# Kernel tuning notes

Hardware: AMD Instinct MI355X
Metric: run time of the kernel (lower is better)

The kernel has to match this reference:

```python
import jax, jax.numpy as jnp
import numpy as np

MAX_FLOW = 80.0
STEPS = 200
STEP_SIZE = 10.0
EPS = 1e-5
NOISE_STD = 0.05
GRAD_CLIP = 0.03


def _energy(flow, img1, img2, log_weights):
    # flow: (B,2,H,W), img1/img2: (B,3,H,W); returns per-sample energy (B,)
    _, _, H, W = img1.shape
    flow = flow * MAX_FLOW
    img1 = (img1 + 1.0) / 2.0
    img2 = (img2 + 1.0) / 2.0
    A = jnp.sum((img1 - img2) ** 2, axis=1)                       # (B,H,W)
    data_term = jnp.sum(jnp.sqrt(A + EPS), axis=(1, 2))           # (B,)
    # kernel_dx/_dy are per-channel [-1,1] finite differences -> slicing
    dx = flow[:, :, :, 1:] - flow[:, :, :, :-1]                   # (B,2,H,W-1)
    dy = flow[:, :, 1:, :] - flow[:, :, :-1, :]                   # (B,2,H-1,W)
    Bx = jnp.pad(jnp.sum(dx ** 2, axis=1), ((0, 0), (0, 0), (0, 1)))
    By = jnp.pad(jnp.sum(dy ** 2, axis=1), ((0, 0), (0, 1), (0, 0)))
    smooth_term = jnp.sum(jnp.sqrt(Bx + By + EPS), axis=(1, 2))   # (B,)
    out = jnp.exp(log_weights[0]) * data_term + jnp.exp(log_weights[1]) * smooth_term
    return out / (H * W)


def _langevin_sample(init, img2, log_weights, key):
    # 200-step Langevin MCMC: noise inject, clamp, energy grad, clipped update, clamp
    def energy_sum(x):
        flow, img1 = x[:, :2], x[:, 2:]
        return jnp.sum(_energy(flow, img1, img2, log_weights))

    grad_fn = jax.grad(energy_sum)

    def step(x, k):
        noise = NOISE_STD * jax.random.normal(k, x.shape, x.dtype)
        x = jnp.clip(x + noise, -1.0, 1.0)
        g = jnp.clip(grad_fn(x), -GRAD_CLIP, GRAD_CLIP)
        x = jnp.clip(x - STEP_SIZE * g, -1.0, 1.0)
        return x, None

    keys = jax.random.split(key, STEPS)
    x, _ = jax.lax.scan(step, init, keys)
    return x


def setup_inputs() -> dict:
    key = jax.random.key(0)
    k1, k2, k3, k4 = jax.random.split(key, 4)
    B, H, W = 8, 384, 512
    target1 = jax.random.normal(k1, (B, 2, H, W), dtype=jnp.float32)
    input1 = jax.random.uniform(k2, (B, 3, H, W), dtype=jnp.float32)
    input2 = jax.random.uniform(k3, (B, 3, H, W), dtype=jnp.float32)
    init = jax.random.uniform(k4, (B, 5, H, W), dtype=jnp.float32) * 2.0 - 1.0
    log_weights = jnp.ones((2,), dtype=jnp.float32)
    return {"target1": target1, "input1": input1, "input2": input2,
            "init": init, "log_weights": log_weights}


def reference(target1, input1, input2, init, log_weights):
    flow_pos = target1 / MAX_FLOW
    img1_pos = input1 * 2.0 - 1.0
    img2 = input2 * 2.0 - 1.0
    # negative samples via Langevin MCMC; detached as in the torch module
    neg = jax.lax.stop_gradient(_langevin_sample(init, img2, log_weights, jax.random.key(1)))
    flow_neg, img1_neg = neg[:, :2], neg[:, 2:]
    pos_energy = _energy(flow_pos, img1_pos, img2, log_weights)
    neg_energy = _energy(flow_neg, img1_neg, img2, log_weights)
    energies = jnp.stack([pos_energy, neg_energy])  # (2,B)
    return energies, flow_neg * MAX_FLOW, (img1_neg + 1.0) / 2.0
```

## Files before the change

### kernel.cpp

```cpp
#include <hip/hip_runtime.h>
#include <math.h>

#define HH 384
#define WW 512
#define HW 196608
#define HHW 98304
#define CHW 983040
#define NTOT 7864320
#define FLOW_N 3145728
#define OUT_FLOW_OFF 16
#define OUT_IMG_OFF (16 + FLOW_N)
#define EPS_F 1e-5f
#define EPS_S (1e-5f / 6400.0f)
#define INV_HW (1.0f/196608.0f)

__device__ __forceinline__ float rsq_f(float x)  { return __builtin_amdgcn_rsqf(x); }
__device__ __forceinline__ float ln_f(float x)   { return 0.69314718055994531f * __builtin_amdgcn_logf(x); }
__device__ __forceinline__ float sqrt_f(float x) { return __builtin_amdgcn_sqrtf(x); }

__host__ __device__ __forceinline__ void tf2x32(unsigned k0, unsigned k1,
                                                unsigned x0, unsigned x1,
                                                unsigned& o0, unsigned& o1) {
  const unsigned ks2 = k0 ^ k1 ^ 0x1BD11BDAu;
  x0 += k0; x1 += k1;
#define TFR(r) x0 += x1; x1 = (x1 << (r)) | (x1 >> (32 - (r))); x1 ^= x0;
  TFR(13) TFR(15) TFR(26) TFR(6)
  x0 += k1;  x1 += ks2 + 1u;
  TFR(17) TFR(29) TFR(16) TFR(24)
  x0 += ks2; x1 += k0 + 2u;
  TFR(13) TFR(15) TFR(26) TFR(6)
  x0 += k0;  x1 += k1 + 3u;
  TFR(17) TFR(29) TFR(16) TFR(24)
  x0 += k1;  x1 += ks2 + 4u;
  TFR(13) TFR(15) TFR(26) TFR(6)
  x0 += ks2; x1 += k0 + 5u;
#undef TFR
  o0 = x0; o1 = x1;
}

__device__ __forceinline__ float noise_from_bits(unsigned bits) {
  const float LO = -0.99999994f;
  float f = __uint_as_float((bits >> 9) | 0x3F800000u) - 1.0f;
  float u = fmaxf(LO, f * 2.0f + LO);
  float w = -ln_f((1.0f - u) * (1.0f + u));
  float p;
  if (w < 5.0f) {
    w -= 2.5f;
    p = 2.81022636e-08f;
    p = p * w + 3.43273939e-07f;
    p = p * w + -3.5233877e-06f;
    p = p * w + -4.39150654e-06f;
    p = p * w + 0.00021858087f;
    p = p * w + -0.00125372503f;
    p = p * w + -0.00417768164f;
    p = p * w + 0.246640727f;
    p = p * w + 1.50140941f;
  } else {
    w = sqrt_f(w) - 3.0f;
    p = -0.000200214257f;
    p = p * w + 0.000100950558f;
    p = p * w + 0.00134934322f;
    p = p * w + -0.00367342844f;
    p = p * w + 0.00573950773f;
    p = p * w + -0.0076224613f;
    p = p * w + 0.00943887047f;
    p = p * w + 1.00167406f;
    p = p * w + 2.83297682f;
  }
  float z = 1.4142135623730951f * (p * u);
  return 0.05f * z;
}

__device__ __forceinline__ float upd(float x, float g) {
  g = fminf(fmaxf(g, -0.03f), 0.03f);
  return fminf(fmaxf(x - 10.0f * g, -1.0f), 1.0f);
}

__device__ __forceinline__ void noise_store2(float* dst, const float xn[2],
                                             unsigned ka, unsigned kb, unsigned idx0) {
  unsigned o0, o1, o2, o3;
  tf2x32(ka, kb, 0u, idx0, o0, o1);
  tf2x32(ka, kb, 0u, idx0 + 1u, o2, o3);
  float r0 = fminf(fmaxf(xn[0] + noise_from_bits(o0 ^ o1), -1.0f), 1.0f);
  float r1 = fminf(fmaxf(xn[1] + noise_from_bits(o2 ^ o3), -1.0f), 1.0f);
  *(float2*)dst = make_float2(r0, r1);
}

__global__ void k_init(double* acc, float* sw, const float* lw) {
  int t = threadIdx.x;
  if (t < 32) acc[t] = 0.0;
  if (t == 32) {
    sw[0] = expf(lw[0]) * INV_HW * 0.5f;
    sw[1] = expf(lw[1]) * INV_HW * 80.0f;
  }
}

__global__ __launch_bounds__(256) void k_noise0(const float* __restrict__ init,
    float* __restrict__ Y, unsigned ka, unsigned kb) {
  int idx = blockIdx.x * 256 + threadIdx.x;
  unsigned o0, o1;
  tf2x32(ka, kb, 0u, (unsigned)idx, o0, o1);
  float nz = noise_from_bits(o0 ^ o1);
  Y[idx] = fminf(fmaxf(init[idx] + nz, -1.0f), 1.0f);
}

template <bool FINAL>
__global__ __launch_bounds__(256, 8) void k_step2(const float* __restrict__ X,
    float* __restrict__ Y, const float* __restrict__ in2,
    const float* __restrict__ sw, unsigned ka, unsigned kb) {
  int tid = blockIdx.x * 256 + threadIdx.x;
  int b = tid / HHW;
  int q = tid - b * HHW;
  int p = q * 2;
  int h = p >> 9, w = p & 511;
  float s0 = sw[0], s1 = sw[1];
  const float* F0 = X + b * CHW;
  const float* F1 = F0 + HW;
  const bool wpos = (w > 0), wend = (w == 510);
  const bool hpos = (h > 0), hlast = (h == 383);

  float cf[2][3], fm1[2], dw[2][2], dwm1[2], uf[2][3];
  {
    float2 a0 = *(const float2*)(F0 + p);
    float2 a1 = *(const float2*)(F1 + p);
    cf[0][0] = a0.x; cf[0][1] = a0.y;
    cf[1][0] = a1.x; cf[1][1] = a1.y;
    cf[0][2] = wend ? cf[0][1] : F0[p + 2];
    cf[1][2] = wend ? cf[1][1] : F1[p + 2];
    fm1[0] = wpos ? F0[p - 1] : cf[0][0];
    fm1[1] = wpos ? F1[p - 1] : cf[1][0];
    if (!hlast) {
      float2 d0 = *(const float2*)(F0 + p + WW);
      float2 d1 = *(const float2*)(F1 + p + WW);
      dw[0][0] = d0.x; dw[0][1] = d0.y;
      dw[1][0] = d1.x; dw[1][1] = d1.y;
      dwm1[0] = wpos ? F0[p + WW - 1] : fm1[0];
      dwm1[1] = wpos ? F1[p + WW - 1] : fm1[1];
    } else {
#pragma unroll
      for (int c = 0; c < 2; ++c) {
        dw[c][0] = cf[c][0]; dw[c][1] = cf[c][1];
        dwm1[c] = fm1[c];
      }
    }
    if (hpos) {
      float2 u0 = *(const float2*)(F0 + p - WW);
      float2 u1 = *(const float2*)(F1 + p - WW);
      uf[0][0] = u0.x; uf[0][1] = u0.y;
      uf[1][0] = u1.x; uf[1][1] = u1.y;
      uf[0][2] = wend ? uf[0][1] : F0[p - WW + 2];
      uf[1][2] = wend ? uf[1][1] : F1[p - WW + 2];
    } else {
#pragma unroll
      for (int c = 0; c < 2; ++c)
        for (int j = 0; j < 3; ++j) uf[c][j] = cf[c][j];
    }
  }

  float dxc[2][2], dyc[2][2], invSc[2], dxu[2][2], dyu[2][2], invSu[2];
  float dxl[2], dyl[2], invSL;
#pragma unroll
  for (int j = 0; j < 2; ++j) {
#pragma unroll
    for (int c = 0; c < 2; ++c) {
      dxc[c][j] = cf[c][j + 1] - cf[c][j];
      dyc[c][j] = dw[c][j] - cf[c][j];
      dxu[c][j] = uf[c][j + 1] - uf[c][j];
      dyu[c][j] = cf[c][j] - uf[c][j];
    }
    invSc[j] = rsq_f(dxc[0][j]*dxc[0][j] + dxc[1][j]*dxc[1][j]
                   + dyc[0][j]*dyc[0][j] + dyc[1][j]*dyc[1][j] + EPS_S);
    invSu[j] = rsq_f(dxu[0][j]*dxu[0][j] + dxu[1][j]*dxu[1][j]
                   + dyu[0][j]*dyu[0][j] + dyu[1][j]*dyu[1][j] + EPS_S);
  }
  dxl[0] = cf[0][0] - fm1[0];  dxl[1] = cf[1][0] - fm1[1];
  dyl[0] = dwm1[0] - fm1[0];   dyl[1] = dwm1[1] - fm1[1];
  invSL = rsq_f(dxl[0]*dxl[0] + dxl[1]*dxl[1]
              + dyl[0]*dyl[0] + dyl[1]*dyl[1] + EPS_S);

  float xnF[2][2];
#pragma unroll
  for (int j = 0; j < 2; ++j) {
#pragma unroll
    for (int c = 0; c < 2; ++c) {
      float g = -(dxc[c][j] + dyc[c][j]) * invSc[j];
      if (j == 0) { if (wpos) g += dxl[c] * invSL; }
      else        { g += dxc[c][0] * invSc[0]; }
      if (hpos)   { g += dyu[c][j] * invSu[j]; }
      xnF[c][j] = upd(cf[c][j], g * s1);
    }
  }

  const float* XI = F0 + 2 * HW;
  const float* I2 = in2 + b * 3 * HW;
  float xv[3][2], dI[3][2];
#pragma unroll
  for (int c = 0; c < 3; ++c) {
    float2 xvv = *(const float2*)(XI + c * HW + p);
    float2 ivv = *(const float2*)(I2 + c * HW + p);
    xv[c][0] = xvv.x; xv[c][1] = xvv.y;
    dI[c][0] = (xvv.x + 1.0f) * 0.5f - ((ivv.x * 2.0f - 1.0f) + 1.0f) * 0.5f;
    dI[c][1] = (xvv.y + 1.0f) * 0.5f - ((ivv.y * 2.0f - 1.0f) + 1.0f) * 0.5f;
  }
  float xnI[3][2];
#pragma unroll
  for (int j = 0; j < 2; ++j) {
    float A = dI[0][j]*dI[0][j] + dI[1][j]*dI[1][j] + dI[2][j]*dI[2][j];
    float sI = s0 * rsq_f(A + EPS_F);
#pragma unroll
    for (int c = 0; c < 3; ++c) xnI[c][j] = upd(xv[c][j], dI[c][j] * sI);
  }

  if (!FINAL) {
    int base = b * CHW + p;
    noise_store2(Y + base,      xnF[0], ka, kb, (unsigned)base);
    noise_store2(Y + base + HW, xnF[1], ka, kb, (unsigned)(base + HW));
#pragma unroll
    for (int c = 0; c < 3; ++c)
      noise_store2(Y + base + (2 + c) * HW, xnI[c], ka, kb,
                   (unsigned)(base + (2 + c) * HW));
  } else {
    float* outF = Y + OUT_FLOW_OFF + b * 2 * HW;
    *(float2*)(outF + p)      = make_float2(xnF[0][0]*80.f, xnF[0][1]*80.f);
    *(float2*)(outF + HW + p) = make_float2(xnF[1][0]*80.f, xnF[1][1]*80.f);
    float* outI = Y + OUT_IMG_OFF + b * 3 * HW;
#pragma unroll
    for (int c = 0; c < 3; ++c)
      *(float2*)(outI + c * HW + p) = make_float2((xnI[c][0]+1.f)*0.5f,
                                                  (xnI[c][1]+1.f)*0.5f);
  }
}

__device__ __forceinline__ void block_acc2(double v0, double v1, double* a0, double* a1) {
  for (int off = 32; off > 0; off >>= 1) {
    v0 += __shfl_down(v0, off, 64);
    v1 += __shfl_down(v1, off, 64);
  }
  __shared__ double s0m[4], s1m[4];
  int lane = threadIdx.x & 63, wv = threadIdx.x >> 6;
  if (lane == 0) { s0m[wv] = v0; s1m[wv] = v1; }
  __syncthreads();
  if (threadIdx.x == 0) {
    atomicAdd(a0, s0m[0] + s0m[1] + s0m[2] + s0m[3]);
    atomicAdd(a1, s1m[0] + s1m[1] + s1m[2] + s1m[3]);
  }
}

__global__ __launch_bounds__(256) void k_pos_energy(const float* __restrict__ t1,
    const float* __restrict__ in1, const float* __restrict__ in2,
    double* __restrict__ acc) {
  int blk = blockIdx.x;
  int b = blk / 96;
  int local = blk - b * 96;
  const float* T0 = t1 + b * 2 * HW;
  const float* T1 = T0 + HW;
  const float* I1 = in1 + b * 3 * HW;
  const float* I2 = in2 + b * 3 * HW;
  double data = 0.0, smooth = 0.0;
  for (int it = 0; it < 8; ++it) {
    int p = (local * 8 + it) * 256 + threadIdx.x;
    int h = p >> 9, w = p & 511;
    float f00 = (T0[p] / 80.0f) * 80.0f;
    float f10 = (T1[p] / 80.0f) * 80.0f;
    float dx0 = 0, dx1 = 0, dy0 = 0, dy1 = 0;
    if (w < 511) { dx0 = (T0[p+1]/80.0f)*80.0f - f00;  dx1 = (T1[p+1]/80.0f)*80.0f - f10; }
    if (h < 383) { dy0 = (T0[p+WW]/80.0f)*80.0f - f00; dy1 = (T1[p+WW]/80.0f)*80.0f - f10; }
    smooth += (double)sqrtf(dx0*dx0 + dx1*dx1 + dy0*dy0 + dy1*dy1 + EPS_F);
    float d0 = ((I1[p]*2.0f-1.0f)+1.0f)*0.5f        - ((I2[p]*2.0f-1.0f)+1.0f)*0.5f;
    float d1 = ((I1[p+HW]*2.0f-1.0f)+1.0f)*0.5f     - ((I2[p+HW]*2.0f-1.0f)+1.0f)*0.5f;
    float d2 = ((I1[p+2*HW]*2.0f-1.0f)+1.0f)*0.5f   - ((I2[p+2*HW]*2.0f-1.0f)+1.0f)*0.5f;
    data += (double)sqrtf(d0*d0 + d1*d1 + d2*d2 + EPS_F);
  }
  block_acc2(data, smooth, &acc[b], &acc[8 + b]);
}

__global__ __launch_bounds__(256) void k_neg_energy(const float* __restrict__ out,
    const float* __restrict__ in2, double* __restrict__ acc) {
  int blk = blockIdx.x;
  int b = blk / 96;
  int local = blk - b * 96;
  const float* F0 = out + OUT_FLOW_OFF + b * 2 * HW;
  const float* F1 = F0 + HW;
  const float* I = out + OUT_IMG_OFF + b * 3 * HW;
  const float* I2 = in2 + b * 3 * HW;
  double data = 0.0, smooth = 0.0;
  for (int it = 0; it < 8; ++it) {
    int p = (local * 8 + it) * 256 + threadIdx.x;
    int h = p >> 9, w = p & 511;
    float f00 = F0[p], f10 = F1[p];
    float dx0 = 0, dx1 = 0, dy0 = 0, dy1 = 0;
    if (w < 511) { dx0 = F0[p + 1] - f00;  dx1 = F1[p + 1] - f10; }
    if (h < 383) { dy0 = F0[p + WW] - f00; dy1 = F1[p + WW] - f10; }
    smooth += (double)sqrtf(dx0*dx0 + dx1*dx1 + dy0*dy0 + dy1*dy1 + EPS_F);
    float d0 = I[p]        - ((I2[p]*2.0f-1.0f)+1.0f)*0.5f;
    float d1 = I[p+HW]     - ((I2[p+HW]*2.0f-1.0f)+1.0f)*0.5f;
    float d2 = I[p+2*HW]   - ((I2[p+2*HW]*2.0f-1.0f)+1.0f)*0.5f;
    data += (double)sqrtf(d0*d0 + d1*d1 + d2*d2 + EPS_F);
  }
  block_acc2(data, smooth, &acc[16 + b], &acc[24 + b]);
}

__global__ void k_finalize(const double* __restrict__ acc,
                           const float* __restrict__ lw, float* __restrict__ out) {
  int t = threadIdx.x;
  if (t < 16) {
    int b = t & 7, neg = t >> 3;
    double data   = acc[neg * 16 + b];
    double smooth = acc[neg * 16 + 8 + b];
    double e0 = exp((double)lw[0]), e1 = exp((double)lw[1]);
    out[t] = (float)((e0 * data + e1 * smooth) / 196608.0);
  }
}

extern "C" void kernel_launch(void* const* d_in, const int* in_sizes, int n_in,
                              void* d_out, int out_size, void* d_ws, size_t ws_size,
                              hipStream_t stream) {
  const float* t1  = (const float*)d_in[0];
  const float* in1 = (const float*)d_in[1];
  const float* in2 = (const float*)d_in[2];
  const float* init = (const float*)d_in[3];
  const float* lw  = (const float*)d_in[4];
  float* out = (float*)d_out;

  double* acc = (double*)d_ws;
  float* sw = (float*)((char*)d_ws + 256);
  size_t need = 2048 + (size_t)NTOT * sizeof(float);
  float* bufA = (ws_size >= need) ? (float*)((char*)d_ws + 2048)
                                  : (float*)d_in[3];
  float* bufE = out + OUT_FLOW_OFF;

  unsigned K0[200], K1[200];
  for (int t = 0; t < 200; ++t) tf2x32(0u, 1u, 0u, (unsigned)t, K0[t], K1[t]);

  k_init<<<1, 64, 0, stream>>>(acc, sw, lw);
  k_pos_energy<<<8 * 96, 256, 0, stream>>>(t1, in1, in2, acc);
  k_noise0<<<NTOT / 256, 256, 0, stream>>>(init, bufE, K0[0], K1[0]);
  for (int t = 0; t < 199; ++t) {
    const float* src = (t % 2 == 0) ? bufE : bufA;
    float* dst       = (t % 2 == 0) ? bufA : bufE;
    k_step2<false><<<8 * HHW / 256, 256, 0, stream>>>(src, dst, in2, sw,
                                                      K0[t + 1], K1[t + 1]);
  }
  k_step2<true><<<8 * HHW / 256, 256, 0, stream>>>(bufA, out, in2, sw, 0u, 0u);
  k_neg_energy<<<8 * 96, 256, 0, stream>>>(out, in2, acc);
  k_finalize<<<1, 64, 0, stream>>>(acc, lw, out);
}
```

Baseline: 5.519 ms.

## Split pointwise image channels into a single fused 200-step kernel

The image channels' energy gradient is purely per-pixel, so all 200 Langevin steps for those three channels now run inside one kernel that keeps the values in registers. Only the two flow channels, which need a stencil, still ping-pong through global memory with one launch per step. This removes most of the per-step global traffic, which previously covered five channels plus in2. The image kernel runs long per thread with serial RNG work, and the ws fallback now writes to the output flow region.

```diff
diff --git a/kernel.cpp b/kernel.cpp
--- a/kernel.cpp
+++ b/kernel.cpp
@@ -76,13 +76,16 @@
   return fminf(fmaxf(x - 10.0f * g, -1.0f), 1.0f);
 }
 
+__device__ __forceinline__ float noise_at(unsigned ka, unsigned kb, unsigned idx) {
+  unsigned o0, o1;
+  tf2x32(ka, kb, 0u, idx, o0, o1);
+  return noise_from_bits(o0 ^ o1);
+}
+
 __device__ __forceinline__ void noise_store2(float* dst, const float xn[2],
                                              unsigned ka, unsigned kb, unsigned idx0) {
-  unsigned o0, o1, o2, o3;
-  tf2x32(ka, kb, 0u, idx0, o0, o1);
-  tf2x32(ka, kb, 0u, idx0 + 1u, o2, o3);
-  float r0 = fminf(fmaxf(xn[0] + noise_from_bits(o0 ^ o1), -1.0f), 1.0f);
-  float r1 = fminf(fmaxf(xn[1] + noise_from_bits(o2 ^ o3), -1.0f), 1.0f);
+  float r0 = fminf(fmaxf(xn[0] + noise_at(ka, kb, idx0), -1.0f), 1.0f);
+  float r1 = fminf(fmaxf(xn[1] + noise_at(ka, kb, idx0 + 1u), -1.0f), 1.0f);
   *(float2*)dst = make_float2(r0, r1);
 }
 
@@ -95,26 +98,27 @@
   }
 }
 
-__global__ __launch_bounds__(256) void k_noise0(const float* __restrict__ init,
+__global__ __launch_bounds__(256) void k_fnoise0(const float* __restrict__ init,
     float* __restrict__ Y, unsigned ka, unsigned kb) {
-  int idx = blockIdx.x * 256 + threadIdx.x;
-  unsigned o0, o1;
-  tf2x32(ka, kb, 0u, (unsigned)idx, o0, o1);
-  float nz = noise_from_bits(o0 ^ o1);
-  Y[idx] = fminf(fmaxf(init[idx] + nz, -1.0f), 1.0f);
+  int e = blockIdx.x * 256 + threadIdx.x;
+  int b = e / (2 * HW);
+  int r = e - b * 2 * HW;
+  int orig = b * CHW + r;
+  float nz = noise_at(ka, kb, (unsigned)orig);
+  Y[e] = fminf(fmaxf(init[orig] + nz, -1.0f), 1.0f);
 }
 
 template <bool FINAL>
-__global__ __launch_bounds__(256, 8) void k_step2(const float* __restrict__ X,
-    float* __restrict__ Y, const float* __restrict__ in2,
-    const float* __restrict__ sw, unsigned ka, unsigned kb) {
+__global__ __launch_bounds__(256, 8) void k_fstep(const float* __restrict__ X,
+    float* __restrict__ Y, const float* __restrict__ sw,
+    unsigned ka, unsigned kb) {
   int tid = blockIdx.x * 256 + threadIdx.x;
   int b = tid / HHW;
   int q = tid - b * HHW;
   int p = q * 2;
   int h = p >> 9, w = p & 511;
-  float s0 = sw[0], s1 = sw[1];
-  const float* F0 = X + b * CHW;
+  float s1 = sw[1];
+  const float* F0 = X + b * 2 * HW;
   const float* F1 = F0 + HW;
   const bool wpos = (w > 0), wend = (w == 510);
   const bool hpos = (h > 0), hlast = (h == 383);
@@ -191,44 +195,58 @@
     }
   }
 
-  const float* XI = F0 + 2 * HW;
-  const float* I2 = in2 + b * 3 * HW;
-  float xv[3][2], dI[3][2];
-#pragma unroll
-  for (int c = 0; c < 3; ++c) {
-    float2 xvv = *(const float2*)(XI + c * HW + p);
-    float2 ivv = *(const float2*)(I2 + c * HW + p);
-    xv[c][0] = xvv.x; xv[c][1] = xvv.y;
-    dI[c][0] = (xvv.x + 1.0f) * 0.5f - ((ivv.x * 2.0f - 1.0f) + 1.0f) * 0.5f;
-    dI[c][1] = (xvv.y + 1.0f) * 0.5f - ((ivv.y * 2.0f - 1.0f) + 1.0f) * 0.5f;
-  }
-  float xnI[3][2];
-#pragma unroll
-  for (int j = 0; j < 2; ++j) {
-    float A = dI[0][j]*dI[0][j] + dI[1][j]*dI[1][j] + dI[2][j]*dI[2][j];
-    float sI = s0 * rsq_f(A + EPS_F);
-#pragma unroll
-    for (int c = 0; c < 3; ++c) xnI[c][j] = upd(xv[c][j], dI[c][j] * sI);
-  }
-
   if (!FINAL) {
-    int base = b * CHW + p;
-    noise_store2(Y + base,      xnF[0], ka, kb, (unsigned)base);
-    noise_store2(Y + base + HW, xnF[1], ka, kb, (unsigned)(base + HW));
-#pragma unroll
-    for (int c = 0; c < 3; ++c)
-      noise_store2(Y + base + (2 + c) * HW, xnI[c], ka, kb,
-                   (unsigned)(base + (2 + c) * HW));
+    int nbase = b * CHW + p;
+    int sb = b * 2 * HW + p;
+    noise_store2(Y + sb,      xnF[0], ka, kb, (unsigned)nbase);
+    noise_store2(Y + sb + HW, xnF[1], ka, kb, (unsigned)(nbase + HW));
   } else {
     float* outF = Y + OUT_FLOW_OFF + b * 2 * HW;
     *(float2*)(outF + p)      = make_float2(xnF[0][0]*80.f, xnF[0][1]*80.f);
     *(float2*)(outF + HW + p) = make_float2(xnF[1][0]*80.f, xnF[1][1]*80.f);
-    float* outI = Y + OUT_IMG_OFF + b * 3 * HW;
-#pragma unroll
-    for (int c = 0; c < 3; ++c)
-      *(float2*)(outI + c * HW + p) = make_float2((xnI[c][0]+1.f)*0.5f,
-                                                  (xnI[c][1]+1.f)*0.5f);
-  }
+  }
+}
+
+__global__ __launch_bounds__(256, 8) void k_img(const float* __restrict__ init,
+    const float* __restrict__ in2, const float* __restrict__ sw,
+    float* __restrict__ out) {
+  __shared__ unsigned Kl[400];
+  int tid = threadIdx.x;
+  if (tid < 200) {
+    unsigned a, bb;
+    tf2x32(0u, 1u, 0u, (unsigned)tid, a, bb);
+    Kl[2 * tid] = a; Kl[2 * tid + 1] = bb;
+  }
+  __syncthreads();
+  int g = blockIdx.x * 256 + tid;
+  int b = g / HW;
+  int p = g - b * HW;
+  float s0 = sw[0];
+  unsigned base = (unsigned)(b * CHW + 2 * HW + p);
+  float x0 = init[base], x1 = init[base + HW], x2 = init[base + 2 * HW];
+  const float* I2 = in2 + b * 3 * HW + p;
+  float i0 = ((I2[0] * 2.0f - 1.0f) + 1.0f) * 0.5f;
+  float i1 = ((I2[HW] * 2.0f - 1.0f) + 1.0f) * 0.5f;
+  float i2v = ((I2[2 * HW] * 2.0f - 1.0f) + 1.0f) * 0.5f;
+
+  for (int t = 0; t < 200; ++t) {
+    unsigned ka = Kl[2 * t], kb = Kl[2 * t + 1];
+    x0 = fminf(fmaxf(x0 + noise_at(ka, kb, base), -1.0f), 1.0f);
+    x1 = fminf(fmaxf(x1 + noise_at(ka, kb, base + HW), -1.0f), 1.0f);
+    x2 = fminf(fmaxf(x2 + noise_at(ka, kb, base + 2 * HW), -1.0f), 1.0f);
+    float d0 = (x0 + 1.0f) * 0.5f - i0;
+    float d1 = (x1 + 1.0f) * 0.5f - i1;
+    float d2 = (x2 + 1.0f) * 0.5f - i2v;
+    float A = d0*d0 + d1*d1 + d2*d2;
+    float sI = s0 * rsq_f(A + EPS_F);
+    x0 = upd(x0, d0 * sI);
+    x1 = upd(x1, d1 * sI);
+    x2 = upd(x2, d2 * sI);
+  }
+  float* outI = out + OUT_IMG_OFF + b * 3 * HW + p;
+  outI[0]      = (x0 + 1.0f) * 0.5f;
+  outI[HW]     = (x1 + 1.0f) * 0.5f;
+  outI[2 * HW] = (x2 + 1.0f) * 0.5f;
 }
 
 __device__ __forceinline__ void block_acc2(double v0, double v1, double* a0, double* a1) {
@@ -324,24 +342,28 @@
 
   double* acc = (double*)d_ws;
   float* sw = (float*)((char*)d_ws + 256);
-  size_t need = 2048 + (size_t)NTOT * sizeof(float);
-  float* bufA = (ws_size >= need) ? (float*)((char*)d_ws + 2048)
-                                  : (float*)d_in[3];
-  float* bufE = out + OUT_FLOW_OFF;
+  float* bufFA = (float*)((char*)d_ws + 2048);
+  size_t need = 2048 + 2 * (size_t)FLOW_N * sizeof(float);
+  float* bufFB = (ws_size >= need) ? bufFA + FLOW_N
+                                   : out + OUT_FLOW_OFF;
 
   unsigned K0[200], K1[200];
   for (int t = 0; t < 200; ++t) tf2x32(0u, 1u, 0u, (unsigned)t, K0[t], K1[t]);
 
   k_init<<<1, 64, 0, stream>>>(acc, sw, lw);
   k_pos_energy<<<8 * 96, 256, 0, stream>>>(t1, in1, in2, acc);
-  k_noise0<<<NTOT / 256, 256, 0, stream>>>(init, bufE, K0[0], K1[0]);
+
+  k_fnoise0<<<FLOW_N / 256, 256, 0, stream>>>(init, bufFB, K0[0], K1[0]);
   for (int t = 0; t < 199; ++t) {
-    const float* src = (t % 2 == 0) ? bufE : bufA;
-    float* dst       = (t % 2 == 0) ? bufA : bufE;
-    k_step2<false><<<8 * HHW / 256, 256, 0, stream>>>(src, dst, in2, sw,
+    const float* src = (t % 2 == 0) ? bufFB : bufFA;
+    float* dst       = (t % 2 == 0) ? bufFA : bufFB;
+    k_fstep<false><<<8 * HHW / 256, 256, 0, stream>>>(src, dst, sw,
                                                       K0[t + 1], K1[t + 1]);
   }
-  k_step2<true><<<8 * HHW / 256, 256, 0, stream>>>(bufA, out, in2, sw, 0u, 0u);
+  k_fstep<true><<<8 * HHW / 256, 256, 0, stream>>>(bufFA, out, sw, 0u, 0u);
+
+  k_img<<<8 * HW / 256, 256, 0, stream>>>(init, in2, sw, out);
+
   k_neg_energy<<<8 * 96, 256, 0, stream>>>(out, in2, acc);
   k_finalize<<<1, 64, 0, stream>>>(acc, lw, out);
 }
```

After: 5.322 ms. -3.6%, faster.
